# Kernel optimization log

Hardware: AMD Instinct MI355X
Metric: run time of the kernel (lower is better)

The kernel has to match this reference:

```python
import jax, jax.numpy as jnp
import numpy as np

B, T, D = 8, 8192, 768
H, HD = 12, 64            # heads, head_dim
Q_STRIDE = 4              # flattened 2x2 q pooling
WINDOW = 64               # flattened mask-unit size after pooling
SCALE = HD ** -0.5


def setup_inputs() -> dict:
    key = jax.random.key(0)
    ks = jax.random.split(key, 5)
    return {
        "embeddings": jax.random.normal(ks[0], (B, T, D), jnp.float32),
        "qkv_w": jax.random.normal(ks[1], (3 * D, D), jnp.float32) * 0.02,
        "qkv_b": jax.random.normal(ks[2], (3 * D,), jnp.float32) * 0.02,
        "proj_w": jax.random.normal(ks[3], (D, D), jnp.float32) * 0.02,
        "proj_b": jax.random.normal(ks[4], (D,), jnp.float32) * 0.02,
    }


def reference(embeddings, qkv_w, qkv_b, proj_w, proj_b):
    b, t, _ = embeddings.shape
    nw = t // (Q_STRIDE * WINDOW)          # number of mask-unit windows
    seq = t // nw                           # tokens per window (pre q-pool)
    # qkv: [b, t, 3D] -> [b, seq, nw, 3, H, HD] (windows are interleaved along tokens)
    qkv = (embeddings @ qkv_w.T + qkv_b).reshape(b, seq, nw, 3, H, HD)
    qkv = jnp.transpose(qkv, (3, 0, 4, 2, 1, 5))  # [3, b, H, nw, seq, HD]
    q, k, v = qkv[0], qkv[1], qkv[2]
    # q max-pool over stride groups (interleaved split of seq)
    q = q.reshape(b, H, nw, Q_STRIDE, seq // Q_STRIDE, HD).max(axis=3)
    attn = jax.nn.softmax(
        jnp.einsum("bhwqd,bhwkd->bhwqk", q * SCALE, k), axis=-1
    )  # [b, H, nw, q_len, seq]
    out = jnp.einsum("bhwqk,bhwkd->bhwqd", attn, v)  # [b, H, nw, q_len, HD]
    out = jnp.transpose(out, (0, 3, 2, 1, 4)).reshape(b, -1, H * HD)
    out = out @ proj_w.T + proj_b
    return out, attn
```

## Files before the change

kernel.cpp:

```cpp
#include <hip/hip_runtime.h>
#include <hip/hip_bf16.h>


typedef float  f32x4  __attribute__((ext_vector_type(4)));
typedef __bf16 bf16x8 __attribute__((ext_vector_type(8)));

__device__ __forceinline__ unsigned short f2bf(float f) {
  unsigned int u = __float_as_uint(f);
  u += 0x7fffu + ((u >> 16) & 1u);
  return (unsigned short)(u >> 16);
}
__device__ __forceinline__ float bf2f(unsigned short b) {
  return __uint_as_float(((unsigned int)b) << 16);
}

#define GLOAD_LDS16(gptr, lptr) __builtin_amdgcn_global_load_lds( \
    (const __attribute__((address_space(1))) void*)(gptr),        \
    (__attribute__((address_space(3))) void*)(lptr), 16, 0, 0)

__global__ void cvt_bf16(const float* __restrict__ src,
                         unsigned short* __restrict__ dst, int n4) {
  int i = blockIdx.x * blockDim.x + threadIdx.x;
  const int stride = gridDim.x * blockDim.x;
  for (; i < n4; i += stride) {
    const float4 v = ((const float4*)src)[i];
    ushort4 o;
    o.x = f2bf(v.x); o.y = f2bf(v.y); o.z = f2bf(v.z); o.w = f2bf(v.w);
    ((ushort4*)dst)[i] = o;
  }
}

template <int OUT_BF16>
__global__ __launch_bounds__(512, 2) void gemm256(
    const unsigned short* __restrict__ A, const unsigned short* __restrict__ B,
    const float* __restrict__ bias, void* __restrict__ Cout,
    int M, int N, int K) {
  extern __shared__ char lds[];

  const int tid  = threadIdx.x;
  const int lane = tid & 63;
  const int wid  = tid >> 6;
  const int g16  = (lane >> 4) & 3;
  const int l15  = lane & 15;
  const int wm   = wid >> 2;
  const int wn   = wid & 3;

  const int nbn = N >> 8;
  const int wg  = (blockIdx.x & 7) * ((int)gridDim.x >> 3) + (blockIdx.x >> 3);
  const size_t bm = (size_t)(wg / nbn) << 8;
  const size_t bn = (size_t)(wg % nbn) << 8;

  const int NT = K >> 6;

  const int srow = tid >> 2;
  const int csel = (((tid & 3) ^ ((tid >> 3) & 3)) << 3);
  const int ldst = wid * 1024;
  const unsigned short* pA0 = A + (bm + srow) * (size_t)K;
  const unsigned short* pA1 = pA0 + (size_t)128 * K;
  const unsigned short* pB0 = B + (bn + srow) * (size_t)K;
  const unsigned short* pB1 = pB0 + (size_t)128 * K;

#define STAGE(p0, p1, kcol, regbase)                                   \
  do {                                                                 \
    GLOAD_LDS16((p0) + (kcol) + csel, lds + (regbase) + ldst);         \
    GLOAD_LDS16((p1) + (kcol) + csel, lds + (regbase) + 8192 + ldst);  \
  } while (0)

  const int s16  = ((g16 ^ ((l15 >> 1) & 3)) << 4);
  const int offA = (wm * 128 + l15) * 64 + s16;
  const int offB = (wn * 64 + l15) * 64 + s16;

  f32x4 acc[8][4];
  const f32x4 zero4 = {0.f, 0.f, 0.f, 0.f};
#pragma unroll
  for (int i = 0; i < 8; ++i)
#pragma unroll
    for (int j = 0; j < 4; ++j) acc[i][j] = zero4;

#define READ_A(par, kk, rh)                                              \
  { const char* rb = lds + (par) * 32768 + (kk) * 16384 + offA + (rh) * 4096; \
    af[0] = *(const bf16x8*)(rb);                                        \
    af[1] = *(const bf16x8*)(rb + 1024);                                 \
    af[2] = *(const bf16x8*)(rb + 2048);                                 \
    af[3] = *(const bf16x8*)(rb + 3072); }
#define READ_B(par, kk)                                                  \
  { const char* rb = lds + 65536 + (par) * 32768 + (kk) * 16384 + offB;  \
    bfv[0] = *(const bf16x8*)(rb);                                       \
    bfv[1] = *(const bf16x8*)(rb + 1024);                                \
    bfv[2] = *(const bf16x8*)(rb + 2048);                                \
    bfv[3] = *(const bf16x8*)(rb + 3072); }
#define MFMA16(rh)                                                       \
  _Pragma("unroll") for (int q = 0; q < 4; ++q)                          \
  _Pragma("unroll") for (int c = 0; c < 4; ++c)                          \
    acc[(rh) * 4 + q][c] = __builtin_amdgcn_mfma_f32_16x16x32_bf16(      \
        af[q], bfv[c], acc[(rh) * 4 + q][c], 0, 0, 0);
#define BAR() __builtin_amdgcn_s_barrier()
#define SCB() __builtin_amdgcn_sched_barrier(0)
#define VMCNT8() { asm volatile("s_waitcnt vmcnt(8)"); SCB(); }

  STAGE(pA0, pA1, 0, 0);
  STAGE(pB0, pB1, 0, 65536);
  STAGE(pA0, pA1, 32, 16384);
  STAGE(pB0, pB1, 32, 65536 + 16384);
  {
    const int k1 = (NT > 1 ? 64 : 0);
    STAGE(pA0, pA1, k1, 32768);
    STAGE(pB0, pB1, k1, 65536 + 32768);
  }
  VMCNT8();
  BAR(); SCB();

  for (int t = 0; t < NT; ++t) {
    const int par  = t & 1;
    const int parn = par ^ 1;
    const int kc1  = (t + 1 < NT ? t + 1 : NT - 1) * 64;
    const int kc2  = (t + 2 < NT ? t + 2 : NT - 1) * 64;
    bf16x8 af[4], bfv[4];

    READ_A(par, 0, 0); READ_B(par, 0);
    STAGE(pA0, pA1, kc1 + 32, parn * 32768 + 16384);
    BAR(); SCB();
    __builtin_amdgcn_s_setprio(1); MFMA16(0); __builtin_amdgcn_s_setprio(0);
    SCB(); BAR();

    READ_A(par, 0, 1);
    STAGE(pB0, pB1, kc1 + 32, 65536 + parn * 32768 + 16384);
    VMCNT8();
    BAR(); SCB();
    __builtin_amdgcn_s_setprio(1); MFMA16(1); __builtin_amdgcn_s_setprio(0);
    SCB(); BAR();

    READ_A(par, 1, 0); READ_B(par, 1);
    STAGE(pA0, pA1, kc2, par * 32768);
    BAR(); SCB();
    __builtin_amdgcn_s_setprio(1); MFMA16(0); __builtin_amdgcn_s_setprio(0);
    SCB(); BAR();

    READ_A(par, 1, 1);
    STAGE(pB0, pB1, kc2, 65536 + par * 32768);
    VMCNT8();
    BAR(); SCB();
    __builtin_amdgcn_s_setprio(1); MFMA16(1); __builtin_amdgcn_s_setprio(0);
    SCB(); BAR();
  }

#pragma unroll
  for (int ai = 0; ai < 8; ++ai) {
    const size_t row0 = bm + wm * 128 + (ai >> 2) * 64 + (ai & 3) * 16 + g16 * 4;
#pragma unroll
    for (int c = 0; c < 4; ++c) {
      const size_t col = bn + wn * 64 + c * 16 + l15;
      const float bv = bias[col];
#pragma unroll
      for (int r = 0; r < 4; ++r) {
        const float v = acc[ai][c][r] + bv;
        const size_t idx = (row0 + r) * N + col;
        if (OUT_BF16) ((unsigned short*)Cout)[idx] = f2bf(v);
        else          ((float*)Cout)[idx] = v;
      }
    }
  }
#undef STAGE
#undef READ_A
#undef READ_B
#undef MFMA16
#undef BAR
#undef SCB
#undef VMCNT8
}

template <int OUT_BF16>
__global__ __launch_bounds__(256) void gemm_bt(
    const unsigned short* __restrict__ A, const unsigned short* __restrict__ B,
    const float* __restrict__ bias, void* __restrict__ Cout,
    int M, int N, int K) {
  __shared__ unsigned short As[128 * 64];
  __shared__ unsigned short Bs[128 * 64];

  const int tid  = threadIdx.x;
  const int lane = tid & 63;
  const int wid  = tid >> 6;
  const int g16  = lane >> 4;
  const int l15  = lane & 15;
  const int bm = blockIdx.x * 128;
  const int bn = blockIdx.y * 128;
  const int wr = (wid >> 1) * 64;
  const int wc = (wid & 1) * 64;

  const f32x4 zero4 = {0.f, 0.f, 0.f, 0.f};
  f32x4 acc[4][4];
#pragma unroll
  for (int m = 0; m < 4; ++m)
#pragma unroll
    for (int n = 0; n < 4; ++n) acc[m][n] = zero4;

  const int flatBase = tid * 16;

  for (int kt = 0; kt < K; kt += 64) {
#pragma unroll
    for (int c = 0; c < 4; ++c) {
      const int flat = c * 4096 + flatBase;
      const int row  = flat >> 7;
      const int cole = (flat & 127) >> 1;
      const unsigned short* ga = A + (size_t)(bm + row) * K + kt + cole;
      const unsigned short* gb = B + (size_t)(bn + row) * K + kt + cole;
      GLOAD_LDS16(ga, (char*)As + c * 4096 + wid * 1024);
      GLOAD_LDS16(gb, (char*)Bs + c * 4096 + wid * 1024);
    }
    __syncthreads();
#pragma unroll
    for (int kk = 0; kk < 2; ++kk) {
      bf16x8 af[4], bfv[4];
#pragma unroll
      for (int m = 0; m < 4; ++m)
        af[m] = *(const bf16x8*)((const char*)As +
                 ((wr + m * 16 + l15) * 64 + kk * 32 + g16 * 8) * 2);
#pragma unroll
      for (int n = 0; n < 4; ++n)
        bfv[n] = *(const bf16x8*)((const char*)Bs +
                 ((wc + n * 16 + l15) * 64 + kk * 32 + g16 * 8) * 2);
#pragma unroll
      for (int m = 0; m < 4; ++m)
#pragma unroll
        for (int n = 0; n < 4; ++n)
          acc[m][n] = __builtin_amdgcn_mfma_f32_16x16x32_bf16(af[m], bfv[n],
                                                              acc[m][n], 0, 0, 0);
    }
    __syncthreads();
  }

#pragma unroll
  for (int n = 0; n < 4; ++n) {
    const int col = bn + wc + n * 16 + l15;
    const float bv = bias[col];
#pragma unroll
    for (int m = 0; m < 4; ++m) {
      const int rowb = bm + wr + m * 16 + g16 * 4;
#pragma unroll
      for (int r = 0; r < 4; ++r) {
        const float v = acc[m][n][r] + bv;
        const size_t idx = (size_t)(rowb + r) * N + col;
        if (OUT_BF16) ((unsigned short*)Cout)[idx] = f2bf(v);
        else          ((float*)Cout)[idx] = v;
      }
    }
  }
}

__global__ __launch_bounds__(256) void attn_kernel(
    const unsigned short* __restrict__ qkv,
    float* __restrict__ attn_out,
    unsigned short* __restrict__ Xws) {
  __shared__ unsigned short smem[32768];
  char* KP = (char*)smem;
  char* VT = (char*)(smem + 16384);

  const int tid  = threadIdx.x;
  const int lane = tid & 63;
  const int wid  = tid >> 6;
  const int g16  = lane >> 4;
  const int l15  = lane & 15;

  const int bid = blockIdx.x;
  const int w = bid & 31;
  const int h = (bid >> 5) % 12;
  const int b = bid / 384;

  {
    const int s0 = tid >> 3;
    const int part = tid & 7;
#pragma unroll
    for (int p = 0; p < 8; ++p) {
      const int s = s0 + p * 32;
      const size_t gbase =
          ((size_t)b * 8192 + (size_t)s * 32 + w) * 2304 + h * 64 + part * 8;
      int4 kv = *(const int4*)(qkv + gbase + 768);
      *(int4*)(KP + ((s * 128 + part * 16) ^ ((s & 7) << 4))) = kv;
      int4 vv = *(const int4*)(qkv + gbase + 1536);
      const unsigned short* pv = (const unsigned short*)&vv;
#pragma unroll
      for (int j = 0; j < 8; ++j) {
        const int d = part * 8 + j;
        *(unsigned short*)(VT + ((d * 512 + s * 2) ^ ((d & 7) << 4))) = pv[j];
      }
    }
  }

  union BU { unsigned short u[8]; bf16x8 v; };
  BU aq0, aq1;
  {
    const int qrow = wid * 16 + l15;
    float q0[8], q1[8];
#pragma unroll
    for (int j = 0; j < 8; ++j) { q0[j] = -1e30f; q1[j] = -1e30f; }
#pragma unroll
    for (int g = 0; g < 4; ++g) {
      const size_t gbase =
          ((size_t)b * 8192 + (size_t)(g * 64 + qrow) * 32 + w) * 2304 +
          h * 64 + g16 * 8;
      int4 a = *(const int4*)(qkv + gbase);
      int4 c = *(const int4*)(qkv + gbase + 32);
      const unsigned short* pa = (const unsigned short*)&a;
      const unsigned short* pc = (const unsigned short*)&c;
#pragma unroll
      for (int j = 0; j < 8; ++j) {
        q0[j] = fmaxf(q0[j], bf2f(pa[j]));
        q1[j] = fmaxf(q1[j], bf2f(pc[j]));
      }
    }
#pragma unroll
    for (int j = 0; j < 8; ++j) {
      aq0.u[j] = (unsigned short)(__float_as_uint(q0[j]) >> 16);
      aq1.u[j] = (unsigned short)(__float_as_uint(q1[j]) >> 16);
    }
  }

  __syncthreads();

  f32x4 sacc[16];
  const f32x4 zero4 = {0.f, 0.f, 0.f, 0.f};
#pragma unroll
  for (int t = 0; t < 16; ++t) sacc[t] = zero4;
#pragma unroll
  for (int t = 0; t < 16; ++t) {
    const int srow = t * 16 + l15;
    bf16x8 bk0 = *(const bf16x8*)(KP + ((srow * 128 + 0  + g16 * 16) ^ ((srow & 7) << 4)));
    bf16x8 bk1 = *(const bf16x8*)(KP + ((srow * 128 + 64 + g16 * 16) ^ ((srow & 7) << 4)));
    sacc[t] = __builtin_amdgcn_mfma_f32_16x16x32_bf16(aq0.v, bk0, sacc[t], 0, 0, 0);
    sacc[t] = __builtin_amdgcn_mfma_f32_16x16x32_bf16(aq1.v, bk1, sacc[t], 0, 0, 0);
  }

  float inv_[4];
#pragma unroll
  for (int r = 0; r < 4; ++r) {
    float m = -1e30f;
#pragma unroll
    for (int t = 0; t < 16; ++t) { sacc[t][r] *= 0.125f; m = fmaxf(m, sacc[t][r]); }
#pragma unroll
    for (int off = 1; off < 16; off <<= 1) m = fmaxf(m, __shfl_xor(m, off, 64));
    float ssum = 0.f;
#pragma unroll
    for (int t = 0; t < 16; ++t) {
      float e = expf(sacc[t][r] - m);
      sacc[t][r] = e;
      ssum += e;
    }
#pragma unroll
    for (int off = 1; off < 16; off <<= 1) ssum += __shfl_xor(ssum, off, 64);
    inv_[r] = 1.f / ssum;
  }

  {
    float* ab = attn_out + ((size_t)bid * 64 + wid * 16) * 256;
#pragma unroll
    for (int t = 0; t < 16; ++t)
#pragma unroll
      for (int r = 0; r < 4; ++r) {
        const float p = sacc[t][r] * inv_[r];
        sacc[t][r] = p;
        ab[(size_t)(g16 * 4 + r) * 256 + t * 16 + l15] = p;
      }
  }

  __syncthreads();

  {
    char* PW = KP + wid * 8192;
#pragma unroll
    for (int t = 0; t < 16; ++t)
#pragma unroll
      for (int r = 0; r < 4; ++r) {
        const int row = g16 * 4 + r;
        *(unsigned short*)(PW + ((row * 512 + (t * 16 + l15) * 2) ^ ((row & 7) << 4))) =
            f2bf(sacc[t][r]);
      }
  }

  f32x4 oacc[4];
#pragma unroll
  for (int n = 0; n < 4; ++n) oacc[n] = zero4;
  {
    const char* PR = KP + wid * 8192;
#pragma unroll
    for (int kc = 0; kc < 8; ++kc) {
      bf16x8 pa = *(const bf16x8*)(PR + ((l15 * 512 + kc * 64 + g16 * 16) ^ ((l15 & 7) << 4)));
#pragma unroll
      for (int n = 0; n < 4; ++n) {
        const int d = n * 16 + l15;
        bf16x8 vv = *(const bf16x8*)(VT + ((d * 512 + kc * 64 + g16 * 16) ^ ((d & 7) << 4)));
        oacc[n] = __builtin_amdgcn_mfma_f32_16x16x32_bf16(pa, vv, oacc[n], 0, 0, 0);
      }
    }
  }

#pragma unroll
  for (int n = 0; n < 4; ++n)
#pragma unroll
    for (int r = 0; r < 4; ++r) {
      const int qi = wid * 16 + g16 * 4 + r;
      Xws[((size_t)b * 2048 + qi * 32 + w) * 768 + h * 64 + n * 16 + l15] =
          f2bf(oacc[n][r]);
    }
}

extern "C" void kernel_launch(void* const* d_in, const int* in_sizes, int n_in,
                              void* d_out, int out_size, void* d_ws, size_t ws_size,
                              hipStream_t stream) {
  const float* emb    = (const float*)d_in[0];
  const float* qkv_w  = (const float*)d_in[1];
  const float* qkv_b  = (const float*)d_in[2];
  const float* proj_w = (const float*)d_in[3];
  const float* proj_b = (const float*)d_in[4];
  float* out = (float*)d_out;

  char* ws = (char*)d_ws;
  unsigned short* embB   = (unsigned short*)(ws);
  unsigned short* wqkvB  = (unsigned short*)(ws + 100663296);
  unsigned short* wprojB = (unsigned short*)(ws + 104202240);
  unsigned short* qkvB   = (unsigned short*)(ws + 105381888);
  unsigned short* Xws    = (unsigned short*)(ws + 407371776);

  cvt_bf16<<<4096, 256, 0, stream>>>(emb, embB, 50331648 / 4);
  cvt_bf16<<<1728, 256, 0, stream>>>(qkv_w, wqkvB, 1769472 / 4);
  cvt_bf16<<<576, 256, 0, stream>>>(proj_w, wprojB, 589824 / 4);

  hipFuncSetAttribute(reinterpret_cast<const void*>(&gemm256<1>),
                      hipFuncAttributeMaxDynamicSharedMemorySize, 131072);
  gemm256<1><<<2304, 512, 131072, stream>>>(embB, wqkvB, qkv_b, qkvB,
                                            65536, 2304, 768);

  attn_kernel<<<3072, 256, 0, stream>>>(qkvB, out + 12582912, Xws);

  gemm_bt<0><<<dim3(128, 6), 256, 0, stream>>>(Xws, wprojB, proj_b, out,
                                               16384, 768, 768);
}
```

Before: 489.3 us.

## Make QKV GEMM persistent over N tiles per M row-block

The QKV projection GEMM now launches one 256-row block per M tile (256 blocks), and each block loops over all N tiles and K steps as a single continuous pipeline. The next tile's loads are issued while the previous tile's epilogue runs, and the accumulators are reset between tiles. This removes per-tile prologue/epilogue pipeline bubbles and keeps each A row-block resident in cache across N tiles. The cost is only 256 workgroups, which may underfill the CUs at 2 blocks/CU, and the epilogue stores now sit inside the main loop.

```diff
diff --git a/kernel.cpp b/kernel.cpp
--- a/kernel.cpp
+++ b/kernel.cpp
@@ -31,7 +31,7 @@
 }
 
 template <int OUT_BF16>
-__global__ __launch_bounds__(512, 2) void gemm256(
+__global__ __launch_bounds__(512, 2) void gemm256p(
     const unsigned short* __restrict__ A, const unsigned short* __restrict__ B,
     const float* __restrict__ bias, void* __restrict__ Cout,
     int M, int N, int K) {
@@ -45,25 +45,28 @@
   const int wm   = wid >> 2;
   const int wn   = wid & 3;
 
-  const int nbn = N >> 8;
-  const int wg  = (blockIdx.x & 7) * ((int)gridDim.x >> 3) + (blockIdx.x >> 3);
-  const size_t bm = (size_t)(wg / nbn) << 8;
-  const size_t bn = (size_t)(wg % nbn) << 8;
-
+  const size_t bm = (size_t)blockIdx.x << 8;
   const int NT = K >> 6;
+  const int NB = N >> 8;
+  const int TT = NB * NT;
 
   const int srow = tid >> 2;
   const int csel = (((tid & 3) ^ ((tid >> 3) & 3)) << 3);
   const int ldst = wid * 1024;
-  const unsigned short* pA0 = A + (bm + srow) * (size_t)K;
+  const unsigned short* pA0 = A + (bm + srow) * (size_t)K + csel;
   const unsigned short* pA1 = pA0 + (size_t)128 * K;
-  const unsigned short* pB0 = B + (bn + srow) * (size_t)K;
+  const unsigned short* pB0 = B + (size_t)srow * K + csel;
   const unsigned short* pB1 = pB0 + (size_t)128 * K;
 
-#define STAGE(p0, p1, kcol, regbase)                                   \
-  do {                                                                 \
-    GLOAD_LDS16((p0) + (kcol) + csel, lds + (regbase) + ldst);         \
-    GLOAD_LDS16((p1) + (kcol) + csel, lds + (regbase) + 8192 + ldst);  \
+#define STAGE_A(koff, regbase)                                          \
+  do {                                                                  \
+    GLOAD_LDS16(pA0 + (koff), lds + (regbase) + ldst);                  \
+    GLOAD_LDS16(pA1 + (koff), lds + (regbase) + 8192 + ldst);           \
+  } while (0)
+#define STAGE_B(boff, regbase)                                          \
+  do {                                                                  \
+    GLOAD_LDS16(pB0 + (boff), lds + (regbase) + ldst);                  \
+    GLOAD_LDS16(pB1 + (boff), lds + (regbase) + 8192 + ldst);           \
   } while (0)
 
   const int s16  = ((g16 ^ ((l15 >> 1) & 3)) << 4);
@@ -98,69 +101,86 @@
 #define SCB() __builtin_amdgcn_sched_barrier(0)
 #define VMCNT8() { asm volatile("s_waitcnt vmcnt(8)"); SCB(); }
 
-  STAGE(pA0, pA1, 0, 0);
-  STAGE(pB0, pB1, 0, 65536);
-  STAGE(pA0, pA1, 32, 16384);
-  STAGE(pB0, pB1, 32, 65536 + 16384);
-  {
-    const int k1 = (NT > 1 ? 64 : 0);
-    STAGE(pA0, pA1, k1, 32768);
-    STAGE(pB0, pB1, k1, 65536 + 32768);
-  }
+  int    kk  = 0;
+  int    bnC = 0;
+  int    k1  = 64;
+  int    k2  = 128;
+  size_t rB1 = 0;
+  size_t rB2 = 0;
+
+  STAGE_A(0, 0);
+  STAGE_B(0, 65536);
+  STAGE_A(32, 16384);
+  STAGE_B(32, 65536 + 16384);
+  STAGE_A(64, 32768);
+  STAGE_B(64, 65536 + 32768);
   VMCNT8();
   BAR(); SCB();
 
-  for (int t = 0; t < NT; ++t) {
-    const int par  = t & 1;
+  for (int s = 0; s < TT; ++s) {
+    const int par  = s & 1;
     const int parn = par ^ 1;
-    const int kc1  = (t + 1 < NT ? t + 1 : NT - 1) * 64;
-    const int kc2  = (t + 2 < NT ? t + 2 : NT - 1) * 64;
     bf16x8 af[4], bfv[4];
 
     READ_A(par, 0, 0); READ_B(par, 0);
-    STAGE(pA0, pA1, kc1 + 32, parn * 32768 + 16384);
+    STAGE_A(k1 + 32, parn * 32768 + 16384);
     BAR(); SCB();
     __builtin_amdgcn_s_setprio(1); MFMA16(0); __builtin_amdgcn_s_setprio(0);
     SCB(); BAR();
 
     READ_A(par, 0, 1);
-    STAGE(pB0, pB1, kc1 + 32, 65536 + parn * 32768 + 16384);
+    STAGE_B(rB1 + k1 + 32, 65536 + parn * 32768 + 16384);
     VMCNT8();
     BAR(); SCB();
     __builtin_amdgcn_s_setprio(1); MFMA16(1); __builtin_amdgcn_s_setprio(0);
     SCB(); BAR();
 
     READ_A(par, 1, 0); READ_B(par, 1);
-    STAGE(pA0, pA1, kc2, par * 32768);
+    STAGE_A(k2, par * 32768);
     BAR(); SCB();
     __builtin_amdgcn_s_setprio(1); MFMA16(0); __builtin_amdgcn_s_setprio(0);
     SCB(); BAR();
 
     READ_A(par, 1, 1);
-    STAGE(pB0, pB1, kc2, 65536 + par * 32768);
+    STAGE_B(rB2 + k2, 65536 + par * 32768);
     VMCNT8();
     BAR(); SCB();
     __builtin_amdgcn_s_setprio(1); MFMA16(1); __builtin_amdgcn_s_setprio(0);
     SCB(); BAR();
-  }
-
-#pragma unroll
-  for (int ai = 0; ai < 8; ++ai) {
-    const size_t row0 = bm + wm * 128 + (ai >> 2) * 64 + (ai & 3) * 16 + g16 * 4;
-#pragma unroll
-    for (int c = 0; c < 4; ++c) {
-      const size_t col = bn + wn * 64 + c * 16 + l15;
-      const float bv = bias[col];
-#pragma unroll
-      for (int r = 0; r < 4; ++r) {
-        const float v = acc[ai][c][r] + bv;
-        const size_t idx = (row0 + r) * N + col;
-        if (OUT_BF16) ((unsigned short*)Cout)[idx] = f2bf(v);
-        else          ((float*)Cout)[idx] = v;
-      }
-    }
-  }
-#undef STAGE
+
+    if (kk == NT - 1) {
+#pragma unroll
+      for (int ai = 0; ai < 8; ++ai) {
+        const size_t row0 =
+            bm + wm * 128 + (ai >> 2) * 64 + (ai & 3) * 16 + g16 * 4;
+#pragma unroll
+        for (int c = 0; c < 4; ++c) {
+          const int col = bnC + wn * 64 + c * 16 + l15;
+          const float bv = bias[col];
+#pragma unroll
+          for (int r = 0; r < 4; ++r) {
+            const float v = acc[ai][c][r] + bv;
+            const size_t idx = (row0 + r) * (size_t)N + col;
+            if (OUT_BF16) ((unsigned short*)Cout)[idx] = f2bf(v);
+            else          ((float*)Cout)[idx] = v;
+          }
+          acc[ai][c] = zero4;
+        }
+      }
+      bnC += 256;
+      kk = 0;
+    } else {
+      ++kk;
+    }
+
+    k1 = k2; rB1 = rB2;
+    if (s + 3 < TT) {
+      k2 += 64;
+      if (k2 == K) { k2 = 0; rB2 += (size_t)256 * K; }
+    }
+  }
+#undef STAGE_A
+#undef STAGE_B
 #undef READ_A
 #undef READ_B
 #undef MFMA16
@@ -424,9 +444,9 @@
   cvt_bf16<<<1728, 256, 0, stream>>>(qkv_w, wqkvB, 1769472 / 4);
   cvt_bf16<<<576, 256, 0, stream>>>(proj_w, wprojB, 589824 / 4);
 
-  hipFuncSetAttribute(reinterpret_cast<const void*>(&gemm256<1>),
+  hipFuncSetAttribute(reinterpret_cast<const void*>(&gemm256p<1>),
                       hipFuncAttributeMaxDynamicSharedMemorySize, 131072);
-  gemm256<1><<<2304, 512, 131072, stream>>>(embB, wqkvB, qkv_b, qkvB,
+  gemm256p<1><<<256, 512, 131072, stream>>>(embB, wqkvB, qkv_b, qkvB,
                                             65536, 2304, 768);
 
   attn_kernel<<<3072, 256, 0, stream>>>(qkvB, out + 12582912, Xws);
```

After: 485.4 us. No clear change (-0.8%).
